# Performance work log

Hardware: AMD Instinct MI355X
Metric: run time of the kernel (lower is better)

## Reference

```python
import jax, jax.numpy as jnp
import numpy as np

N_NODES = 50000
N_EDGES = 800000
HIDDEN = 128


def setup_inputs() -> dict:
    key = jax.random.key(0)
    k_h, k_src, k_dst, k_w1, k_w2 = jax.random.split(key, 5)
    h = jax.random.normal(k_h, (N_NODES, HIDDEN), dtype=jnp.float32)
    src = jax.random.randint(k_src, (N_EDGES,), 0, N_NODES, dtype=jnp.int32)
    dst = jax.random.randint(k_dst, (N_EDGES,), 0, N_NODES, dtype=jnp.int32)
    edge_index = jnp.stack([src, dst], axis=0)
    # MLP params (torch Linear: y = x @ W.T + b); store as [in, out] for einsum
    s1 = 1.0 / np.sqrt(2 * HIDDEN)
    s2 = 1.0 / np.sqrt(HIDDEN)
    W1 = jax.random.uniform(k_w1, (2 * HIDDEN, HIDDEN), jnp.float32, -s1, s1)
    b1 = jnp.zeros((HIDDEN,), jnp.float32)
    W2 = jax.random.uniform(k_w2, (HIDDEN, HIDDEN), jnp.float32, -s2, s2)
    b2 = jnp.zeros((HIDDEN,), jnp.float32)
    return {"h": h, "edge_index": edge_index, "W1": W1, "b1": b1, "W2": W2, "b2": b2}


def reference(h, edge_index, W1, b1, W2, b2):
    src, dst = edge_index[0], edge_index[1]
    n = h.shape[0]
    # scatter-add of gathered source features -> agg [N, H]
    agg = jax.ops.segment_sum(h[src], dst, num_segments=n)
    # degree normalization (clamp_min 1)
    deg = jax.ops.segment_sum(jnp.ones_like(dst, dtype=h.dtype), dst, num_segments=n)
    deg = jnp.maximum(deg, 1.0)[:, None]
    agg = agg / deg
    x = jnp.concatenate([h, agg], axis=1)  # [N, 2H]
    x = jax.nn.relu(x @ W1 + b1)
    x = jax.nn.relu(x @ W2 + b2)
    return x
```

## Files before the change

### kernel.cpp

```cpp
#include <hip/hip_runtime.h>

typedef unsigned short u16;
typedef unsigned int u32;
typedef __attribute__((ext_vector_type(8))) short short8;
typedef __attribute__((ext_vector_type(4))) float f32x4;
typedef __attribute__((ext_vector_type(4))) u32 u32x4;

__device__ inline u16 f2bf(float f){ u32 u=__float_as_uint(f); u32 r=((u>>16)&1u)+0x7fffu; return (u16)((u+r)>>16); }

__global__ __launch_bounds__(256) void k_fill_misc(
    const int* __restrict__ src, const int* __restrict__ dst,
    int* __restrict__ cnt, u16* __restrict__ bucket, int nE,
    const float* __restrict__ h, u16* __restrict__ hbf, int nh8,
    const float* __restrict__ w1, const float* __restrict__ w2,
    u16* __restrict__ w1t, u16* __restrict__ w2t){
  int e = blockIdx.x*256 + threadIdx.x;
  if (e < nE){
    int d = dst[e];
    int slot = atomicAdd(&cnt[d], 1);
    if (slot < 128) bucket[(size_t)d*256 + slot] = (u16)src[e];
  }
  if (e < nh8){
    float4 a = *(const float4*)(h + (size_t)e*8);
    float4 b = *(const float4*)(h + (size_t)e*8 + 4);
    u32x4 p;
    p.x = (u32)f2bf(a.x) | ((u32)f2bf(a.y)<<16);
    p.y = (u32)f2bf(a.z) | ((u32)f2bf(a.w)<<16);
    p.z = (u32)f2bf(b.x) | ((u32)f2bf(b.y)<<16);
    p.w = (u32)f2bf(b.z) | ((u32)f2bf(b.w)<<16);
    *(u32x4*)(hbf + (size_t)e*8) = p;
  }
  if (e < 256*128){ int k=e>>7, nn=e&127; w1t[nn*256+k]=f2bf(w1[e]); }
  else { int j=e-256*128; if (j<128*128){ int k=j>>7, nn=j&127; w2t[nn*128+k]=f2bf(w2[j]); } }
}

__global__ __launch_bounds__(256) void k_agg(
    const u16* __restrict__ hbf, const int* __restrict__ cnt,
    u32* __restrict__ outw, int n){
  int node = (int)((blockIdx.x*256 + threadIdx.x) >> 6);
  int lane = threadIdx.x & 63;
  if (node >= n) return;
  int c = cnt[node]; if (c > 128) c = 128;
  const u16* bucket = (const u16*)outw + (size_t)node*256;
  float a0=0.f, a1=0.f;
  int nb = c >> 5;
  for (int b=0;b<nb;b++){
    int base = b*32;
    int sidx[32];
    #pragma unroll
    for (int j=0;j<32;j++) sidx[j] = bucket[base+j];
    u32 vv[32];
    #pragma unroll
    for (int j=0;j<32;j++) vv[j] = *(const u32*)(hbf + (size_t)sidx[j]*128 + lane*2);
    #pragma unroll
    for (int j=0;j<32;j++){
      union{u32 u; float f;} lo,hi; lo.u=vv[j]<<16; hi.u=vv[j]&0xffff0000u;
      a0 += lo.f; a1 += hi.f;
    }
  }
  int rem = c & 31;
  if (rem){
    int base = nb*32;
    int sidx[32];
    #pragma unroll
    for (int j=0;j<32;j++) sidx[j] = bucket[base + (j<rem ? j : rem-1)];
    u32 vv[32];
    #pragma unroll
    for (int j=0;j<32;j++) vv[j] = *(const u32*)(hbf + (size_t)sidx[j]*128 + lane*2);
    #pragma unroll
    for (int j=0;j<32;j++){
      float m = (j<rem) ? 1.f : 0.f;
      union{u32 u; float f;} lo,hi; lo.u=vv[j]<<16; hi.u=vv[j]&0xffff0000u;
      a0 += m*lo.f; a1 += m*hi.f;
    }
  }
  float inv = 1.f/(float)(c>0?c:1);
  outw[(size_t)node*128 + 64 + lane] = (u32)f2bf(a0*inv) | ((u32)f2bf(a1*inv)<<16);
}

__global__ __launch_bounds__(256, 4) void k_mlp(
    const u16* __restrict__ hbf, const u32* __restrict__ outw_in,
    const u16* __restrict__ w1t, const u16* __restrict__ w2t,
    const float* __restrict__ b1, const float* __restrict__ b2,
    float* __restrict__ out, int n){
  __shared__ __align__(16) u16 xs[64*264];
  int t = threadIdx.x;
  int node0 = blockIdx.x*64;
  int wave=t>>6, lane=t&63, quad=lane>>4, l16=lane&15;
  int nt0 = wave*2;

  const u16* w1p0 = w1t + (size_t)((nt0  )*16 + l16)*256 + quad*8;
  const u16* w1p1 = w1t + (size_t)((nt0+1)*16 + l16)*256 + quad*8;
  short8 wb1[16];
  #pragma unroll
  for (int ks=0;ks<8;ks++){
    wb1[ks*2+0] = *(const short8*)(w1p0 + ks*32);
    wb1[ks*2+1] = *(const short8*)(w1p1 + ks*32);
  }

  #pragma unroll
  for (int i=0;i<8;i++){
    int idx = i*256 + t;
    int row = idx>>5, c8 = idx&31;
    int node = node0 + row;
    u32x4 v = {0,0,0,0};
    if (node < n){
      if (c8 < 16) v = *(const u32x4*)(hbf + (size_t)node*128 + c8*8);
      else         v = *(const u32x4*)(outw_in + (size_t)node*128 + 64 + (c8-16)*4);
    }
    *(u32x4*)(&xs[row*264 + c8*8]) = v;
  }
  __syncthreads();

  f32x4 acc[4][2];
  #pragma unroll
  for (int m=0;m<4;m++){ acc[m][0]=(f32x4){0,0,0,0}; acc[m][1]=(f32x4){0,0,0,0}; }
  #pragma unroll
  for (int ks=0;ks<8;ks++){
    #pragma unroll
    for (int m=0;m<4;m++){
      short8 a = *(const short8*)(&xs[(m*16+l16)*264 + ks*32 + quad*8]);
      acc[m][0] = __builtin_amdgcn_mfma_f32_16x16x32_bf16(a, wb1[ks*2+0], acc[m][0],0,0,0);
      acc[m][1] = __builtin_amdgcn_mfma_f32_16x16x32_bf16(a, wb1[ks*2+1], acc[m][1],0,0,0);
    }
  }

  const u16* w2p0 = w2t + (size_t)((nt0  )*16 + l16)*128 + quad*8;
  const u16* w2p1 = w2t + (size_t)((nt0+1)*16 + l16)*128 + quad*8;
  short8 wb2[8];
  #pragma unroll
  for (int ks=0;ks<4;ks++){
    wb2[ks*2+0] = *(const short8*)(w2p0 + ks*32);
    wb2[ks*2+1] = *(const short8*)(w2p1 + ks*32);
  }

  __syncthreads();

  float bias0 = b1[(nt0  )*16 + l16];
  float bias1 = b1[(nt0+1)*16 + l16];
  #pragma unroll
  for (int m=0;m<4;m++){
    #pragma unroll
    for (int r=0;r<4;r++){
      int row = m*16 + quad*4 + r;
      float v0 = acc[m][0][r] + bias0; v0 = v0>0.f ? v0 : 0.f;
      float v1 = acc[m][1][r] + bias1; v1 = v1>0.f ? v1 : 0.f;
      xs[row*264 + (nt0  )*16 + l16] = f2bf(v0);
      xs[row*264 + (nt0+1)*16 + l16] = f2bf(v1);
    }
  }
  __syncthreads();

  f32x4 acc2[4][2];
  #pragma unroll
  for (int m=0;m<4;m++){ acc2[m][0]=(f32x4){0,0,0,0}; acc2[m][1]=(f32x4){0,0,0,0}; }
  #pragma unroll
  for (int ks=0;ks<4;ks++){
    #pragma unroll
    for (int m=0;m<4;m++){
      short8 a = *(const short8*)(&xs[(m*16+l16)*264 + ks*32 + quad*8]);
      acc2[m][0] = __builtin_amdgcn_mfma_f32_16x16x32_bf16(a, wb2[ks*2+0], acc2[m][0],0,0,0);
      acc2[m][1] = __builtin_amdgcn_mfma_f32_16x16x32_bf16(a, wb2[ks*2+1], acc2[m][1],0,0,0);
    }
  }
  float c0 = b2[(nt0  )*16 + l16];
  float c1 = b2[(nt0+1)*16 + l16];
  #pragma unroll
  for (int m=0;m<4;m++){
    #pragma unroll
    for (int r=0;r<4;r++){
      int node = node0 + m*16 + quad*4 + r;
      if (node<n){
        float v0 = acc2[m][0][r]+c0; v0 = v0>0.f?v0:0.f;
        float v1 = acc2[m][1][r]+c1; v1 = v1>0.f?v1:0.f;
        out[(size_t)node*128 + (nt0  )*16 + l16] = v0;
        out[(size_t)node*128 + (nt0+1)*16 + l16] = v1;
      }
    }
  }
}

extern "C" void kernel_launch(void* const* d_in, const int* in_sizes, int n_in,
                              void* d_out, int out_size, void* d_ws, size_t ws_size,
                              hipStream_t stream){
  const float* h  = (const float*)d_in[0];
  const int*   ei = (const int*)d_in[1];
  const float* W1 = (const float*)d_in[2];
  const float* b1 = (const float*)d_in[3];
  const float* W2 = (const float*)d_in[4];
  const float* b2 = (const float*)d_in[5];
  float* out = (float*)d_out;
  u32* outw  = (u32*)d_out;
  int n  = in_sizes[0] / 128;
  int nE = in_sizes[1] / 2;
  const int* srcI = ei;
  const int* dstI = ei + nE;

  char* ws = (char*)d_ws;
  u16* hbf    = (u16*)(ws);
  int* cnt    = (int*)(ws + 12800000);
  u16* w1t    = (u16*)(ws + 13000704);
  u16* w2t    = (u16*)(ws + 13066240);

  hipMemsetAsync(cnt, 0, (size_t)n*sizeof(int), stream);
  int gE = (nE+255)/256;
  k_fill_misc<<<gE, 256, 0, stream>>>(srcI, dstI, cnt, (u16*)outw, nE,
                                      h, hbf, n*16, W1, W2, w1t, w2t);
  k_agg <<<(n+3)/4, 256, 0, stream>>>(hbf, cnt, outw, n);
  k_mlp <<<(n+63)/64, 256, 0, stream>>>(hbf, outw, w1t, w2t, b1, b2, out, n);
}
```

Baseline: 176.3 us.

## Split per-node edge buckets into four sub-buckets to spread atomic contention

Each destination node now has four atomic counters and four 32-slot sub-buckets, chosen by edge index mod 4, so concurrent atomics on the same node spread across four addresses. The aggregation kernel reads all four counts, loops up to the largest sub-bucket count in steps of 4, and gathers 16 rows per iteration with masks. Unlike the old 32-wide unmasked batches, every gather is now masked, and the per-node cap becomes 32 per sub-bucket rather than 128 overall. Iterations follow the largest sub-bucket, so uneven sub-bucket fill adds wasted masked gathers. The counter memset is four times larger.

```diff
diff --git a/kernel.cpp b/kernel.cpp
--- a/kernel.cpp
+++ b/kernel.cpp
@@ -10,15 +10,16 @@
 
 __global__ __launch_bounds__(256) void k_fill_misc(
     const int* __restrict__ src, const int* __restrict__ dst,
-    int* __restrict__ cnt, u16* __restrict__ bucket, int nE,
+    int* __restrict__ cnt4, u16* __restrict__ bucket, int nE,
     const float* __restrict__ h, u16* __restrict__ hbf, int nh8,
     const float* __restrict__ w1, const float* __restrict__ w2,
     u16* __restrict__ w1t, u16* __restrict__ w2t){
   int e = blockIdx.x*256 + threadIdx.x;
   if (e < nE){
     int d = dst[e];
-    int slot = atomicAdd(&cnt[d], 1);
-    if (slot < 128) bucket[(size_t)d*256 + slot] = (u16)src[e];
+    int sub = e & 3;
+    int slot = atomicAdd(&cnt4[d*4 + sub], 1);
+    if (slot < 32) bucket[(size_t)d*256 + sub*32 + slot] = (u16)src[e];
   }
   if (e < nh8){
     float4 a = *(const float4*)(h + (size_t)e*8);
@@ -35,43 +36,41 @@
 }
 
 __global__ __launch_bounds__(256) void k_agg(
-    const u16* __restrict__ hbf, const int* __restrict__ cnt,
+    const u16* __restrict__ hbf, const int* __restrict__ cnt4,
     u32* __restrict__ outw, int n){
   int node = (int)((blockIdx.x*256 + threadIdx.x) >> 6);
   int lane = threadIdx.x & 63;
   if (node >= n) return;
-  int c = cnt[node]; if (c > 128) c = 128;
+  int4 cc = *(const int4*)(cnt4 + (size_t)node*4);
+  int csA[4];
+  csA[0] = cc.x>32?32:cc.x; csA[1] = cc.y>32?32:cc.y;
+  csA[2] = cc.z>32?32:cc.z; csA[3] = cc.w>32?32:cc.w;
+  int c = csA[0]+csA[1]+csA[2]+csA[3];
+  int mx = csA[0]>csA[1]?csA[0]:csA[1];
+  int mx2 = csA[2]>csA[3]?csA[2]:csA[3];
+  if (mx2>mx) mx=mx2;
   const u16* bucket = (const u16*)outw + (size_t)node*256;
   float a0=0.f, a1=0.f;
-  int nb = c >> 5;
-  for (int b=0;b<nb;b++){
-    int base = b*32;
-    int sidx[32];
-    #pragma unroll
-    for (int j=0;j<32;j++) sidx[j] = bucket[base+j];
-    u32 vv[32];
-    #pragma unroll
-    for (int j=0;j<32;j++) vv[j] = *(const u32*)(hbf + (size_t)sidx[j]*128 + lane*2);
-    #pragma unroll
-    for (int j=0;j<32;j++){
-      union{u32 u; float f;} lo,hi; lo.u=vv[j]<<16; hi.u=vv[j]&0xffff0000u;
-      a0 += lo.f; a1 += hi.f;
-    }
-  }
-  int rem = c & 31;
-  if (rem){
-    int base = nb*32;
-    int sidx[32];
-    #pragma unroll
-    for (int j=0;j<32;j++) sidx[j] = bucket[base + (j<rem ? j : rem-1)];
-    u32 vv[32];
-    #pragma unroll
-    for (int j=0;j<32;j++) vv[j] = *(const u32*)(hbf + (size_t)sidx[j]*128 + lane*2);
-    #pragma unroll
-    for (int j=0;j<32;j++){
-      float m = (j<rem) ? 1.f : 0.f;
-      union{u32 u; float f;} lo,hi; lo.u=vv[j]<<16; hi.u=vv[j]&0xffff0000u;
-      a0 += m*lo.f; a1 += m*hi.f;
+  for (int base=0; base<mx; base+=4){
+    int sidx[16]; float msk[16];
+    #pragma unroll
+    for (int s=0;s<4;s++){
+      int cs = csA[s];
+      #pragma unroll
+      for (int j=0;j<4;j++){
+        int slot = base+j;
+        int sc = slot < cs ? slot : (cs>0 ? cs-1 : 0);
+        sidx[s*4+j] = bucket[s*32 + sc];
+        msk[s*4+j]  = (slot < cs) ? 1.f : 0.f;
+      }
+    }
+    u32 vv[16];
+    #pragma unroll
+    for (int k=0;k<16;k++) vv[k] = *(const u32*)(hbf + (size_t)sidx[k]*128 + lane*2);
+    #pragma unroll
+    for (int k=0;k<16;k++){
+      union{u32 u; float f;} lo,hi; lo.u=vv[k]<<16; hi.u=vv[k]&0xffff0000u;
+      a0 += msk[k]*lo.f; a1 += msk[k]*hi.f;
     }
   }
   float inv = 1.f/(float)(c>0?c:1);
@@ -198,14 +197,14 @@
 
   char* ws = (char*)d_ws;
   u16* hbf    = (u16*)(ws);
-  int* cnt    = (int*)(ws + 12800000);
-  u16* w1t    = (u16*)(ws + 13000704);
-  u16* w2t    = (u16*)(ws + 13066240);
-
-  hipMemsetAsync(cnt, 0, (size_t)n*sizeof(int), stream);
+  int* cnt4   = (int*)(ws + 12800000);
+  u16* w1t    = (u16*)(ws + 13600000);
+  u16* w2t    = (u16*)(ws + 13665536);
+
+  hipMemsetAsync(cnt4, 0, (size_t)n*4*sizeof(int), stream);
   int gE = (nE+255)/256;
-  k_fill_misc<<<gE, 256, 0, stream>>>(srcI, dstI, cnt, (u16*)outw, nE,
+  k_fill_misc<<<gE, 256, 0, stream>>>(srcI, dstI, cnt4, (u16*)outw, nE,
                                       h, hbf, n*16, W1, W2, w1t, w2t);
-  k_agg <<<(n+3)/4, 256, 0, stream>>>(hbf, cnt, outw, n);
+  k_agg <<<(n+3)/4, 256, 0, stream>>>(hbf, cnt4, outw, n);
   k_mlp <<<(n+63)/64, 256, 0, stream>>>(hbf, outw, w1t, w2t, b1, b2, out, n);
 }
```

Result: slower. 181.3 us (+2.8%).
